# Kernel optimization log

Measured on AMD Instinct MI355X. Metric: run time of the kernel, lower is better.

Reference implementation:

```python
import jax, jax.numpy as jnp
import numpy as np

B, N, D, P = 8, 64, 256, 256   # batch, nodes, input_features, proj_size_filler (== proj_size_role)
E = N * (N - 1)                # complete directed graph


def _layer_norm(x, g, b, eps=1e-5):
    mu = jnp.mean(x, axis=-1, keepdims=True)
    v = jnp.mean((x - mu) ** 2, axis=-1, keepdims=True)
    return (x - mu) * jax.lax.rsqrt(v + eps) * g + b


def _lin_init(k, fin, fout):
    k1, k2 = jax.random.split(k)
    lim = 1.0 / np.sqrt(fin)
    W = jax.random.uniform(k1, (fin, fout), minval=-lim, maxval=lim, dtype=jnp.float32)
    b = jax.random.uniform(k2, (fout,), minval=-lim, maxval=lim, dtype=jnp.float32)
    return W, b


def setup_inputs() -> dict:
    key = jax.random.key(0)
    ks = jax.random.split(key, 10)
    # complete directed graph, src-major order: node i -> all j != i
    src = np.repeat(np.arange(N), N - 1)
    mesh = np.tile(np.arange(N), (N, 1))
    dst = mesh[~np.eye(N, dtype=bool)].reshape(N, N - 1).ravel()
    edge_index = np.broadcast_to(np.stack([src, dst])[None], (B, 2, E)).copy()
    W_f0, b_f0 = _lin_init(ks[0], 3 * D, D)
    W_f1, b_f1 = _lin_init(ks[1], D, D)
    W_f2, b_f2 = _lin_init(ks[2], D, P)
    W_i0, b_i0 = _lin_init(ks[3], 2 * D + P, D)
    W_i1, b_i1 = _lin_init(ks[4], D, D)
    W_i2, b_i2 = _lin_init(ks[5], D, D)
    return {
        "node_features": jax.random.normal(ks[6], (B, N, D), dtype=jnp.float32),
        "edge_features": jax.random.normal(ks[7], (B, E, D), dtype=jnp.float32),
        "target_node": jax.random.normal(ks[8], (B, D), dtype=jnp.float32),
        "edge_index": jnp.asarray(edge_index, dtype=jnp.int32),
        "W_f0": W_f0, "b_f0": b_f0, "W_f1": W_f1, "b_f1": b_f1, "W_f2": W_f2, "b_f2": b_f2,
        "ln_gamma": jnp.ones((P,), jnp.float32), "ln_beta": jnp.zeros((P,), jnp.float32),
        "W_i0": W_i0, "b_i0": b_i0, "W_i1": W_i1, "b_i1": b_i1, "W_i2": W_i2, "b_i2": b_i2,
    }


def reference(node_features, edge_features, target_node, edge_index,
              W_f0, b_f0, W_f1, b_f1, W_f2, b_f2, ln_gamma, ln_beta,
              W_i0, b_i0, W_i1, b_i1, W_i2, b_i2):
    src = edge_index[:, 0, :]                                   # [B,E]
    dst = edge_index[:, 1, :]                                   # [B,E]
    nf_src = jnp.take_along_axis(node_features, src[..., None], axis=1)  # [B,E,D]
    nf_dst = jnp.take_along_axis(node_features, dst[..., None], axis=1)  # [B,E,D]
    # --- initialization: edge-wise MLP (original calls x.relu() without assignment ->
    # no activation; dropout is eval-mode identity) ---
    h = jnp.concatenate([nf_src, edge_features, nf_dst], axis=-1)        # [B,E,3D]
    h = h @ W_f0 + b_f0
    h = h @ W_f1 + b_f1
    filler = h @ W_f2 + b_f2                                             # [B,E,P]
    # scatter-add of per-edge outer products into node memory; edges are src-major
    # (node i owns edges i*(N-1):(i+1)*(N-1)) so the segment-sum is a block reshape.
    mem = jnp.einsum('bnep,bned->bnpd',
                     filler.reshape(B, N, N - 1, P),
                     nf_dst.reshape(B, N, N - 1, D))                     # [B,N,P,D]
    # --- propagation: complete graph => every pair adjacent => BFS yields only
    # trivial length-1 paths, which collect_long_dependancy ignores (identity). ---
    # --- inference ---
    retrieved = jnp.einsum('bnpd,bd->bnp', mem, target_node)             # [B,N,P]
    retrieved = _layer_norm(retrieved, ln_gamma, ln_beta)
    tgt = jnp.broadcast_to(target_node[:, None, :], (B, N, D))
    z = jnp.concatenate([node_features, retrieved, tgt], axis=-1)        # [B,N,2D+P]
    z = z @ W_i0 + b_i0
    z = z @ W_i1 + b_i1
    z = z @ W_i2 + b_i2                                                  # [B,N,D]
    return z
```

## Files before the change

### kernel.cpp

```cpp
#include <hip/hip_runtime.h>

#define BB 8
#define NN 64
#define DD 256
#define PP 256
#define NE 63
#define EE 4032

__global__ __launch_bounds__(512) void k_edge(const float* __restrict__ nf,
                                              const float* __restrict__ ef,
                                              const int* __restrict__ eidx,
                                              float* __restrict__ conc,
                                              float* __restrict__ Svec,
                                              const float* __restrict__ tgt) {
    __shared__ float s_sh[NE];
    __shared__ int src_sh[NE];
    __shared__ int dst_sh[NE];
    __shared__ float Psh[8 * 768];
    int bn = blockIdx.x;
    int b = bn >> 6, n = bn & 63;
    int tid = threadIdx.x;
    int lane = tid & 63;
    int h = tid >> 6;

    if (tid < NE) {
        const int* srcp = eidx + (size_t)b * 2 * EE + n * NE;
        src_sh[tid] = srcp[tid];
        dst_sh[tid] = srcp[EE + tid];
    }
    __syncthreads();

    const float4* nf4  = (const float4*)nf;
    const float4* tgt4 = (const float4*)(tgt + (size_t)b * DD);
    float4 c4 = tgt4[lane];

    int eA0 = h * 8, eA1 = min(NE, h * 8 + 8);
    for (int e = eA0; e < eA1; ++e) {
        int d = dst_sh[e];
        float4 a4 = nf4[(size_t)((b << 6) + d) * 64 + lane];
        float p = a4.x * c4.x + a4.y * c4.y + a4.z * c4.z + a4.w * c4.w;
#pragma unroll
        for (int off = 32; off; off >>= 1) p += __shfl_down(p, off, 64);
        if (lane == 0) s_sh[e] = p;
    }
    __syncthreads();

    if (tid < 64) {
        float v = (tid < NE) ? s_sh[tid] : 0.f;
#pragma unroll
        for (int off = 32; off; off >>= 1) v += __shfl_down(v, off, 64);
        if (tid == 0) Svec[bn] = v;
    }

    const float4* ef4 = (const float4*)ef;
    size_t efbase = ((size_t)b * EE + (size_t)n * NE) * 64 + lane;
    size_t nfbase = (size_t)(b << 6) * 64 + lane;
    float4 at = {0,0,0,0}, aus = {0,0,0,0}, aud = {0,0,0,0};
#pragma unroll 4
    for (int e = eA0; e < eA1; ++e) {
        float sv = s_sh[e];
        float4 fe = ef4[efbase + (size_t)e * 64];
        float4 fs = nf4[nfbase + (size_t)src_sh[e] * 64];
        float4 fd = nf4[nfbase + (size_t)dst_sh[e] * 64];
        at.x += sv * fe.x; at.y += sv * fe.y; at.z += sv * fe.z; at.w += sv * fe.w;
        aus.x += sv * fs.x; aus.y += sv * fs.y; aus.z += sv * fs.z; aus.w += sv * fs.w;
        aud.x += sv * fd.x; aud.y += sv * fd.y; aud.z += sv * fd.z; aud.w += sv * fd.w;
    }
    float4* Pf4 = (float4*)Psh;
    Pf4[(size_t)(h * 3 + 0) * 64 + lane] = aus;
    Pf4[(size_t)(h * 3 + 1) * 64 + lane] = at;
    Pf4[(size_t)(h * 3 + 2) * 64 + lane] = aud;
    __syncthreads();

    float* o = conc + (size_t)bn * 768;
    for (int i = tid; i < 768; i += 512) {
        float s = 0.f;
#pragma unroll
        for (int hh = 0; hh < 8; ++hh) s += Psh[hh * 768 + i];
        o[i] = s;
    }
}

__global__ __launch_bounds__(1024) void k_mlp(const float* __restrict__ conc,
                                              const float* __restrict__ Svec,
                                              const float* __restrict__ nf,
                                              const float* __restrict__ tgt,
                                              const float* __restrict__ Wf0, const float* __restrict__ bf0,
                                              const float* __restrict__ Wf1, const float* __restrict__ bf1,
                                              const float* __restrict__ Wf2, const float* __restrict__ bf2,
                                              const float* __restrict__ gam, const float* __restrict__ bet,
                                              const float* __restrict__ Wi0, const float* __restrict__ bi0,
                                              const float* __restrict__ Wi1, const float* __restrict__ bi1,
                                              const float* __restrict__ Wi2, const float* __restrict__ bi2,
                                              float* __restrict__ outp) {
    __shared__ float At[768 * 4];
    __shared__ float Zt[768 * 4];
    __shared__ float P[16 * 4 * 256];
    __shared__ float Ht[256 * 4];
    __shared__ float red1[16], red2[16];
    int r0 = blockIdx.x * 4;
    int tid = threadIdx.x;
    int jg = tid & 63;
    int h = tid >> 6;
    int col = tid & 255;
    int r2 = tid >> 8;

    {
        const float* cp = conc + (size_t)(r0 + r2) * 768;
#pragma unroll
        for (int q = 0; q < 3; ++q) {
            int k = col + q * 256;
            At[k * 4 + r2] = cp[k];
        }
        Zt[col * 4 + r2]         = nf[(size_t)(r0 + r2) * DD + col];
        Zt[(512 + col) * 4 + r2] = tgt[(size_t)((r0 + r2) >> 6) * DD + col];
    }
    float Sv = Svec[r0 + r2];
    __syncthreads();

    auto layer = [&](const float* Xt, int K, const float* __restrict__ W,
                     const float* __restrict__ bias, bool scaleS,
                     float* OUTt, bool store) -> float {
        int kpart = K >> 4;
        const float4* Wp = (const float4*)(W + (size_t)(h * kpart) * 256) + jg;
        const float4* Xp = (const float4*)Xt + h * kpart;
        float4 a0 = {0,0,0,0}, a1 = {0,0,0,0}, a2 = {0,0,0,0}, a3 = {0,0,0,0};
#pragma unroll 8
        for (int k = 0; k < kpart; ++k) {
            float4 w = Wp[(size_t)k * 64];
            float4 x = Xp[k];
            a0.x += x.x * w.x; a0.y += x.x * w.y; a0.z += x.x * w.z; a0.w += x.x * w.w;
            a1.x += x.y * w.x; a1.y += x.y * w.y; a1.z += x.y * w.z; a1.w += x.y * w.w;
            a2.x += x.z * w.x; a2.y += x.z * w.y; a2.z += x.z * w.z; a2.w += x.z * w.w;
            a3.x += x.w * w.x; a3.y += x.w * w.y; a3.z += x.w * w.z; a3.w += x.w * w.w;
        }
        float4* Pf4 = (float4*)P;
        Pf4[(size_t)(h * 4 + 0) * 64 + jg] = a0;
        Pf4[(size_t)(h * 4 + 1) * 64 + jg] = a1;
        Pf4[(size_t)(h * 4 + 2) * 64 + jg] = a2;
        Pf4[(size_t)(h * 4 + 3) * 64 + jg] = a3;
        __syncthreads();
        float v = 0.f;
#pragma unroll
        for (int hh = 0; hh < 16; ++hh) v += P[(hh * 4 + r2) * 256 + col];
        v += (scaleS ? Sv : 1.f) * bias[col];
        if (store) {
            OUTt[col * 4 + r2] = v;
        }
        __syncthreads();
        return v;
    };

    layer(At, 768, Wf0, bf0, true, Ht, true);
    layer(Ht, 256, Wf1, bf1, true, Ht, true);
    float v = layer(Ht, 256, Wf2, bf2, true, nullptr, false);

    {
        float s1 = v, s2 = v * v;
#pragma unroll
        for (int off = 32; off; off >>= 1) {
            s1 += __shfl_down(s1, off, 64);
            s2 += __shfl_down(s2, off, 64);
        }
        int wv = (tid >> 6) & 3;
        if ((tid & 63) == 0) { red1[r2 * 4 + wv] = s1; red2[r2 * 4 + wv] = s2; }
        __syncthreads();
        float sum = red1[r2 * 4] + red1[r2 * 4 + 1] + red1[r2 * 4 + 2] + red1[r2 * 4 + 3];
        float sq  = red2[r2 * 4] + red2[r2 * 4 + 1] + red2[r2 * 4 + 2] + red2[r2 * 4 + 3];
        float mu  = sum * (1.f / 256.f);
        float var = sq * (1.f / 256.f) - mu * mu;
        float inv = rsqrtf(var + 1e-5f);
        Zt[(256 + col) * 4 + r2] = (v - mu) * inv * gam[col] + bet[col];
        __syncthreads();
    }

    layer(Zt, 768, Wi0, bi0, false, Ht, true);
    layer(Ht, 256, Wi1, bi1, false, Ht, true);
    float o = layer(Ht, 256, Wi2, bi2, false, nullptr, false);
    outp[(size_t)(r0 + r2) * 256 + col] = o;
}

extern "C" void kernel_launch(void* const* d_in, const int* in_sizes, int n_in,
                              void* d_out, int out_size, void* d_ws, size_t ws_size,
                              hipStream_t stream) {
    const float* nf  = (const float*)d_in[0];
    const float* ef  = (const float*)d_in[1];
    const float* tgt = (const float*)d_in[2];
    const int*   ei  = (const int*)d_in[3];
    const float* Wf0 = (const float*)d_in[4];
    const float* bf0 = (const float*)d_in[5];
    const float* Wf1 = (const float*)d_in[6];
    const float* bf1 = (const float*)d_in[7];
    const float* Wf2 = (const float*)d_in[8];
    const float* bf2 = (const float*)d_in[9];
    const float* gam = (const float*)d_in[10];
    const float* bet = (const float*)d_in[11];
    const float* Wi0 = (const float*)d_in[12];
    const float* bi0 = (const float*)d_in[13];
    const float* Wi1 = (const float*)d_in[14];
    const float* bi1 = (const float*)d_in[15];
    const float* Wi2 = (const float*)d_in[16];
    const float* bi2 = (const float*)d_in[17];
    float* out = (float*)d_out;

    float* Svec = (float*)d_ws;
    float* conc = Svec + 512;

    k_edge<<<BB * NN, 512, 0, stream>>>(nf, ef, ei, conc, Svec, tgt);
    k_mlp<<<(BB * NN) / 4, 1024, 0, stream>>>(conc, Svec, nf, tgt,
                                              Wf0, bf0, Wf1, bf1, Wf2, bf2,
                                              gam, bet, Wi0, bi0, Wi1, bi1, Wi2, bi2,
                                              out);
}
```

Baseline: 144.7 us.

## Convert MLP weights to fp16 and precompute node-target dots in separate kernel

Adds a per-call kernel that converts all six MLP weight matrices to fp16 into workspace. The MLP kernel then streams half-width weights and widens them to fp32 for accumulation, which halves weight bandwidth. The per-node dot products with the target node now come from a small separate kernel instead of being recomputed for every edge. The edge kernel also moves to 1024 threads with 4 edges per wave. In exchange it adds two launches and a conversion pass over about 2.6 MB of weights, and rounding weights to fp16 reduces accuracy.

```diff
diff --git a/kernel.cpp b/kernel.cpp
--- a/kernel.cpp
+++ b/kernel.cpp
@@ -7,16 +7,52 @@
 #define NE 63
 #define EE 4032
 
-__global__ __launch_bounds__(512) void k_edge(const float* __restrict__ nf,
-                                              const float* __restrict__ ef,
-                                              const int* __restrict__ eidx,
-                                              float* __restrict__ conc,
-                                              float* __restrict__ Svec,
-                                              const float* __restrict__ tgt) {
-    __shared__ float s_sh[NE];
+typedef _Float16 half4 __attribute__((ext_vector_type(4)));
+typedef _Float16 half2v __attribute__((ext_vector_type(2)));
+
+__global__ __launch_bounds__(256) void k_wconv(const float* __restrict__ Wf0, const float* __restrict__ Wf1,
+                                               const float* __restrict__ Wf2, const float* __restrict__ Wi0,
+                                               const float* __restrict__ Wi1, const float* __restrict__ Wi2,
+                                               _Float16* __restrict__ o) {
+    int i = (blockIdx.x * 256 + threadIdx.x) * 2;
+    const float* src; int off;
+    if (i < 196608)      { src = Wf0; off = 0; }
+    else if (i < 262144) { src = Wf1; off = 196608; }
+    else if (i < 327680) { src = Wf2; off = 262144; }
+    else if (i < 524288) { src = Wi0; off = 327680; }
+    else if (i < 589824) { src = Wi1; off = 524288; }
+    else                 { src = Wi2; off = 589824; }
+    float2 v = *(const float2*)(src + (i - off));
+    half2v h; h.x = (_Float16)v.x; h.y = (_Float16)v.y;
+    *(half2v*)(o + i) = h;
+}
+
+__global__ __launch_bounds__(64) void k_dot(const float* __restrict__ nf,
+                                            const float* __restrict__ tgt,
+                                            float* __restrict__ dotv) {
+    int row = blockIdx.x;
+    int b = row >> 6;
+    int lane = threadIdx.x;
+    const float4* x4 = (const float4*)(nf + (size_t)row * DD);
+    const float4* t4 = (const float4*)(tgt + (size_t)b * DD);
+    float4 a = x4[lane];
+    float4 c = t4[lane];
+    float acc = a.x * c.x + a.y * c.y + a.z * c.z + a.w * c.w;
+#pragma unroll
+    for (int off = 32; off; off >>= 1) acc += __shfl_down(acc, off, 64);
+    if (lane == 0) dotv[row] = acc;
+}
+
+__global__ __launch_bounds__(1024) void k_edge(const float* __restrict__ nf,
+                                               const float* __restrict__ ef,
+                                               const int* __restrict__ eidx,
+                                               const float* __restrict__ dotv,
+                                               float* __restrict__ conc,
+                                               float* __restrict__ Svec) {
+    __shared__ float s_sh[64];
     __shared__ int src_sh[NE];
     __shared__ int dst_sh[NE];
-    __shared__ float Psh[8 * 768];
+    __shared__ float Psh[16 * 768];
     int bn = blockIdx.x;
     int b = bn >> 6, n = bn & 63;
     int tid = threadIdx.x;
@@ -25,23 +61,11 @@
 
     if (tid < NE) {
         const int* srcp = eidx + (size_t)b * 2 * EE + n * NE;
-        src_sh[tid] = srcp[tid];
-        dst_sh[tid] = srcp[EE + tid];
-    }
-    __syncthreads();
-
-    const float4* nf4  = (const float4*)nf;
-    const float4* tgt4 = (const float4*)(tgt + (size_t)b * DD);
-    float4 c4 = tgt4[lane];
-
-    int eA0 = h * 8, eA1 = min(NE, h * 8 + 8);
-    for (int e = eA0; e < eA1; ++e) {
-        int d = dst_sh[e];
-        float4 a4 = nf4[(size_t)((b << 6) + d) * 64 + lane];
-        float p = a4.x * c4.x + a4.y * c4.y + a4.z * c4.z + a4.w * c4.w;
-#pragma unroll
-        for (int off = 32; off; off >>= 1) p += __shfl_down(p, off, 64);
-        if (lane == 0) s_sh[e] = p;
+        int si = srcp[tid];
+        int di = srcp[EE + tid];
+        src_sh[tid] = si;
+        dst_sh[tid] = di;
+        s_sh[tid] = dotv[(b << 6) + di];
     }
     __syncthreads();
 
@@ -52,12 +76,14 @@
         if (tid == 0) Svec[bn] = v;
     }
 
+    const float4* nf4 = (const float4*)nf;
     const float4* ef4 = (const float4*)ef;
     size_t efbase = ((size_t)b * EE + (size_t)n * NE) * 64 + lane;
     size_t nfbase = (size_t)(b << 6) * 64 + lane;
+    int e0 = h * 4, e1 = min(NE, h * 4 + 4);
     float4 at = {0,0,0,0}, aus = {0,0,0,0}, aud = {0,0,0,0};
 #pragma unroll 4
-    for (int e = eA0; e < eA1; ++e) {
+    for (int e = e0; e < e1; ++e) {
         float sv = s_sh[e];
         float4 fe = ef4[efbase + (size_t)e * 64];
         float4 fs = nf4[nfbase + (size_t)src_sh[e] * 64];
@@ -72,12 +98,11 @@
     Pf4[(size_t)(h * 3 + 2) * 64 + lane] = aud;
     __syncthreads();
 
-    float* o = conc + (size_t)bn * 768;
-    for (int i = tid; i < 768; i += 512) {
+    if (tid < 768) {
         float s = 0.f;
 #pragma unroll
-        for (int hh = 0; hh < 8; ++hh) s += Psh[hh * 768 + i];
-        o[i] = s;
+        for (int hh = 0; hh < 16; ++hh) s += Psh[hh * 768 + tid];
+        conc[(size_t)bn * 768 + tid] = s;
     }
 }
 
@@ -85,13 +110,14 @@
                                               const float* __restrict__ Svec,
                                               const float* __restrict__ nf,
                                               const float* __restrict__ tgt,
-                                              const float* __restrict__ Wf0, const float* __restrict__ bf0,
-                                              const float* __restrict__ Wf1, const float* __restrict__ bf1,
-                                              const float* __restrict__ Wf2, const float* __restrict__ bf2,
+                                              const _Float16* __restrict__ Wh,
+                                              const float* __restrict__ bf0,
+                                              const float* __restrict__ bf1,
+                                              const float* __restrict__ bf2,
                                               const float* __restrict__ gam, const float* __restrict__ bet,
-                                              const float* __restrict__ Wi0, const float* __restrict__ bi0,
-                                              const float* __restrict__ Wi1, const float* __restrict__ bi1,
-                                              const float* __restrict__ Wi2, const float* __restrict__ bi2,
+                                              const float* __restrict__ bi0,
+                                              const float* __restrict__ bi1,
+                                              const float* __restrict__ bi2,
                                               float* __restrict__ outp) {
     __shared__ float At[768 * 4];
     __shared__ float Zt[768 * 4];
@@ -105,6 +131,13 @@
     int col = tid & 255;
     int r2 = tid >> 8;
 
+    const _Float16* Wf0h = Wh;
+    const _Float16* Wf1h = Wh + 196608;
+    const _Float16* Wf2h = Wh + 262144;
+    const _Float16* Wi0h = Wh + 327680;
+    const _Float16* Wi1h = Wh + 524288;
+    const _Float16* Wi2h = Wh + 589824;
+
     {
         const float* cp = conc + (size_t)(r0 + r2) * 768;
 #pragma unroll
@@ -118,21 +151,22 @@
     float Sv = Svec[r0 + r2];
     __syncthreads();
 
-    auto layer = [&](const float* Xt, int K, const float* __restrict__ W,
+    auto layer = [&](const float* Xt, int K, const _Float16* __restrict__ W,
                      const float* __restrict__ bias, bool scaleS,
                      float* OUTt, bool store) -> float {
         int kpart = K >> 4;
-        const float4* Wp = (const float4*)(W + (size_t)(h * kpart) * 256) + jg;
+        const half4* Wp = (const half4*)(W + (size_t)(h * kpart) * 256) + jg;
         const float4* Xp = (const float4*)Xt + h * kpart;
         float4 a0 = {0,0,0,0}, a1 = {0,0,0,0}, a2 = {0,0,0,0}, a3 = {0,0,0,0};
 #pragma unroll 8
         for (int k = 0; k < kpart; ++k) {
-            float4 w = Wp[(size_t)k * 64];
+            half4 wh = Wp[(size_t)k * 64];
             float4 x = Xp[k];
-            a0.x += x.x * w.x; a0.y += x.x * w.y; a0.z += x.x * w.z; a0.w += x.x * w.w;
-            a1.x += x.y * w.x; a1.y += x.y * w.y; a1.z += x.y * w.z; a1.w += x.y * w.w;
-            a2.x += x.z * w.x; a2.y += x.z * w.y; a2.z += x.z * w.z; a2.w += x.z * w.w;
-            a3.x += x.w * w.x; a3.y += x.w * w.y; a3.z += x.w * w.z; a3.w += x.w * w.w;
+            float wx = (float)wh.x, wy = (float)wh.y, wz = (float)wh.z, ww = (float)wh.w;
+            a0.x += x.x * wx; a0.y += x.x * wy; a0.z += x.x * wz; a0.w += x.x * ww;
+            a1.x += x.y * wx; a1.y += x.y * wy; a1.z += x.y * wz; a1.w += x.y * ww;
+            a2.x += x.z * wx; a2.y += x.z * wy; a2.z += x.z * wz; a2.w += x.z * ww;
+            a3.x += x.w * wx; a3.y += x.w * wy; a3.z += x.w * wz; a3.w += x.w * ww;
         }
         float4* Pf4 = (float4*)P;
         Pf4[(size_t)(h * 4 + 0) * 64 + jg] = a0;
@@ -151,9 +185,9 @@
         return v;
     };
 
-    layer(At, 768, Wf0, bf0, true, Ht, true);
-    layer(Ht, 256, Wf1, bf1, true, Ht, true);
-    float v = layer(Ht, 256, Wf2, bf2, true, nullptr, false);
+    layer(At, 768, Wf0h, bf0, true, Ht, true);
+    layer(Ht, 256, Wf1h, bf1, true, Ht, true);
+    float v = layer(Ht, 256, Wf2h, bf2, true, nullptr, false);
 
     {
         float s1 = v, s2 = v * v;
@@ -174,9 +208,9 @@
         __syncthreads();
     }
 
-    layer(Zt, 768, Wi0, bi0, false, Ht, true);
-    layer(Ht, 256, Wi1, bi1, false, Ht, true);
-    float o = layer(Ht, 256, Wi2, bi2, false, nullptr, false);
+    layer(Zt, 768, Wi0h, bi0, false, Ht, true);
+    layer(Ht, 256, Wi1h, bi1, false, Ht, true);
+    float o = layer(Ht, 256, Wi2h, bi2, false, nullptr, false);
     outp[(size_t)(r0 + r2) * 256 + col] = o;
 }
 
@@ -203,12 +237,15 @@
     const float* bi2 = (const float*)d_in[17];
     float* out = (float*)d_out;
 
-    float* Svec = (float*)d_ws;
+    float* dotv = (float*)d_ws;
+    float* Svec = dotv + 512;
     float* conc = Svec + 512;
-
-    k_edge<<<BB * NN, 512, 0, stream>>>(nf, ef, ei, conc, Svec, tgt);
-    k_mlp<<<(BB * NN) / 4, 1024, 0, stream>>>(conc, Svec, nf, tgt,
-                                              Wf0, bf0, Wf1, bf1, Wf2, bf2,
-                                              gam, bet, Wi0, bi0, Wi1, bi1, Wi2, bi2,
-                                              out);
-}
+    _Float16* wh = (_Float16*)(conc + 512 * 768);
+
+    k_wconv<<<655360 / 512, 256, 0, stream>>>(Wf0, Wf1, Wf2, Wi0, Wi1, Wi2, wh);
+    k_dot<<<BB * NN, 64, 0, stream>>>(nf, tgt, dotv);
+    k_edge<<<BB * NN, 1024, 0, stream>>>(nf, ef, ei, dotv, conc, Svec);
+    k_mlp<<<(BB * NN) / 4, 1024, 0, stream>>>(conc, Svec, nf, tgt, wh,
+                                              bf0, bf1, bf2, gam, bet,
+                                              bi0, bi1, bi2, out);
+}
```

New measurement: 143.6 us. No clear change (-0.7%).
